# Performance work log

Measured on AMD Instinct MI355X. Metric: run time of the kernel, lower is better.

The kernel has to match this reference:

```python
import jax, jax.numpy as jnp
import numpy as np

SIZE = (256, 256, 256)   # volume shape (self.size)
N = 65536                # number of Gaussians
DIST = 3.0               # render cutoff distance
WIN = 7                  # static stencil width = 2*ceil(DIST)+1


def setup_inputs() -> dict:
    key = jax.random.key(0)
    k1, k2, k3 = jax.random.split(key, 3)
    # positions inside the volume
    pos = jax.random.uniform(k1, (3, N), minval=1.0, maxval=255.0)
    # per-Gaussian value
    value = jax.random.uniform(k2, (1, N), minval=0.1, maxval=1.0)
    # radii: diagonal radii in [1,3], off-diagonal cross terms ~ 0 (1e-5, as in create_guass)
    rdiag = jax.random.uniform(k3, (3, N), minval=1.0, maxval=3.0)
    off = jnp.full((N,), 1e-5, jnp.float32)
    # layout rows 4:10 -> [rx, rxy, rxz, ry, ryz, rz]
    r = jnp.stack([rdiag[0], off, off, rdiag[1], off, rdiag[2]], axis=0)
    paras = jnp.concatenate([pos, value, r], axis=0)  # [10, N]
    return {
        "paras": paras,
        "distance": jnp.float32(DIST),
        "thredhold": jnp.float32(1e-4),
    }


def _render(paras, distance, thredhold):
    # paras: [10, N] -> position [3,N], value [N], r [6,N]
    pos = paras[:3]
    val = paras[3]
    r = paras[4:]
    D0, D1, D2 = SIZE
    size_arr = jnp.array(SIZE, jnp.int32)

    # static local stencil offsets [W^3, 3]
    offs = jnp.stack(
        jnp.meshgrid(jnp.arange(WIN), jnp.arange(WIN), jnp.arange(WIN), indexing="ij"),
        axis=-1,
    ).reshape(-1, 3).astype(jnp.int32)

    corner = jnp.floor(pos.T).astype(jnp.int32) - (WIN // 2)   # [N, 3]
    vox = corner[:, None, :] + offs[None, :, :]                 # [N, W^3, 3] voxel coords
    d = vox.astype(paras.dtype) - pos.T[:, None, :]             # [N, W^3, 3] voxel - center
    dx, dy, dz = d[..., 0], d[..., 1], d[..., 2]

    rx, rxy, rxz, ry, ryz, rz = r  # each [N]
    # anisotropic quadratic form: diagonal radii + cross terms
    q = (
        (dx / rx[:, None]) ** 2
        + (dy / ry[:, None]) ** 2
        + (dz / rz[:, None]) ** 2
        + rxy[:, None] * dx * dy
        + rxz[:, None] * dx * dz
        + ryz[:, None] * dy * dz
    )
    w = jnp.exp(-0.5 * q)                                       # [N, W^3]

    dist2 = dx * dx + dy * dy + dz * dz
    inb = jnp.all((vox >= 0) & (vox < size_arr), axis=-1)
    mask = inb & (dist2 <= distance * distance) & (w > thredhold)
    contrib = jnp.where(mask, val[:, None] * w, 0.0)

    voxc = jnp.clip(vox, 0, size_arr - 1)
    flat = (voxc[..., 0] * D1 + voxc[..., 1]) * D2 + voxc[..., 2]
    out = jnp.zeros(D0 * D1 * D2, paras.dtype).at[flat.reshape(-1)].add(contrib.reshape(-1))
    return out.reshape(SIZE)


def reference(paras, distance, thredhold):
    return _render(paras, distance, thredhold)
```

## Files before the change

kernel.cpp:

```cpp
#include <hip/hip_runtime.h>

#define D0 256
#define D1 256
#define D2 256
#define NPTS 65536
#define HALF 3

#define TX 32
#define TY 16
#define TZ 16
#define NTILES 2048
#define TILE_VOX (TX * TY * TZ)

#define BLK 512
#define WPB 8
#define CAP 256

#define WS_COUNTS 0
#define WS_PREP   2048
#define WS_LIST   (WS_PREP + NPTS * 12)
#define FULL_INTS  (WS_LIST + NTILES * CAP)
#define WS_LIST_NP 2048
#define SMALL_INTS (WS_LIST_NP + NTILES * CAP)

struct OffTable { unsigned v[256]; };

constexpr OffTable make_table() {
    OffTable t{};
    int m[7] = {9, 4, 1, 0, 0, 1, 4};
    int n = 0;
    for (int i = 0; i < 7; i++)
        for (int j = 0; j < 7; j++)
            for (int k = 0; k < 7; k++)
                if (m[i] + m[j] + m[k] <= 9)
                    t.v[n++] = (unsigned)(i | (j << 8) | (k << 16));
    for (; n < 256; n++)
        t.v[n] = (unsigned)(100 | (100 << 8) | (100 << 16));
    return t;
}

__device__ __constant__ OffTable g_tab = make_table();

struct PP { float fx, fy, fz, val, ix, iy, iz, D, E, F; int pack; };

template<bool PREP>
__device__ __forceinline__ PP load_pt(const float* __restrict__ paras,
                                      const float* __restrict__ prep, int pidx) {
    PP P;
    if constexpr (PREP) {
        const float4* p4 = (const float4*)prep + pidx * 3;
        float4 a = p4[0], b4 = p4[1], c4 = p4[2];
        P.fx = a.x;  P.fy = a.y;  P.fz = a.z;  P.val = a.w;
        P.ix = b4.x; P.iy = b4.y; P.iz = b4.z; P.D = b4.w;
        P.E = c4.x;  P.F = c4.y;  P.pack = __float_as_int(c4.z);
    } else {
        float px = paras[pidx], py = paras[NPTS + pidx], pz = paras[2 * NPTS + pidx];
        P.val = paras[3 * NPTS + pidx];
        float rx  = paras[4 * NPTS + pidx], rxy = paras[5 * NPTS + pidx];
        float rxz = paras[6 * NPTS + pidx], ry  = paras[7 * NPTS + pidx];
        float ryz = paras[8 * NPTS + pidx], rz  = paras[9 * NPTS + pidx];
        int cx = (int)floorf(px) - HALF;
        int cy = (int)floorf(py) - HALF;
        int cz = (int)floorf(pz) - HALF;
        P.fx = (float)cx - px; P.fy = (float)cy - py; P.fz = (float)cz - pz;
        P.ix = __fdividef(1.f, rx); P.iy = __fdividef(1.f, ry);
        P.iz = __fdividef(1.f, rz);
        P.D = rxy; P.E = rxz; P.F = ryz;
        P.pack = (cx + 8) | ((cy + 8) << 10) | ((cz + 8) << 20);
    }
    return P;
}

__global__ __launch_bounds__(256)
void bin_kernel(const float* __restrict__ paras, int* __restrict__ ws,
                float* __restrict__ prep, int do_prep, int list_off) {
    int t = blockIdx.x * 256 + threadIdx.x;
    int p = t >> 3, j = t & 7;

    float px = paras[p], py = paras[NPTS + p], pz = paras[2 * NPTS + p];
    int cx = (int)floorf(px) - HALF;
    int cy = (int)floorf(py) - HALF;
    int cz = (int)floorf(pz) - HALF;

    if (do_prep && j == 0) {
        float val = paras[3 * NPTS + p];
        float rx  = paras[4 * NPTS + p], rxy = paras[5 * NPTS + p];
        float rxz = paras[6 * NPTS + p], ry  = paras[7 * NPTS + p];
        float ryz = paras[8 * NPTS + p], rz  = paras[9 * NPTS + p];
        int pack = (cx + 8) | ((cy + 8) << 10) | ((cz + 8) << 20);
        float4* o = (float4*)prep + p * 3;
        o[0] = make_float4((float)cx - px, (float)cy - py, (float)cz - pz, val);
        o[1] = make_float4(__fdividef(1.f, rx), __fdividef(1.f, ry),
                           __fdividef(1.f, rz), rxy);
        o[2] = make_float4(rxz, ryz, __int_as_float(pack), 0.f);
    }

    int xlo = max(cx, 0), xhi = min(cx + 6, D0 - 1);
    int ylo = max(cy, 0), yhi = min(cy + 6, D1 - 1);
    int zlo = max(cz, 0), zhi = min(cz + 6, D2 - 1);
    int txa = xlo >> 5, txb = xhi >> 5;
    int tya = ylo >> 4, tyb = yhi >> 4;
    int tza = zlo >> 4, tzb = zhi >> 4;

    bool dup = ((j & 1) && txb == txa) ||
               ((j & 2) && tyb == tya) ||
               ((j & 4) && tzb == tza);
    if (!dup) {
        int tx = (j & 1) ? txb : txa;
        int ty = (j & 2) ? tyb : tya;
        int tz = (j & 4) ? tzb : tza;
        int tt = (tx << 8) | (ty << 4) | tz;
        int slot = atomicAdd(&ws[WS_COUNTS + tt], 1);
        if (slot < CAP) ws[list_off + tt * CAP + slot] = p;
    }
}

template<bool PREP>
__global__ __launch_bounds__(512)
void tile_splat(const float* __restrict__ paras,
                const float* __restrict__ prep,
                const float* __restrict__ dist_p,
                const float* __restrict__ thr_p,
                const int* __restrict__ ws, int list_off,
                float* __restrict__ out) {
    __shared__ float acc[TILE_VOX];

    const int b   = blockIdx.x;
    const int tzi = b & 15, tyi = (b >> 4) & 15, txi = b >> 8;
    const int X0 = txi * TX, Y0 = tyi * TY, Z0 = tzi * TZ;
    const int tid = threadIdx.x;
    const int wid = tid >> 6, lane = tid & 63;

    int   oiv[4], ojv[4], okv[4];
    float foi[4], foj[4], fok[4];
#pragma unroll
    for (int t = 0; t < 4; t++) {
        unsigned pk = g_tab.v[t * 64 + lane];
        oiv[t] = pk & 255; ojv[t] = (pk >> 8) & 255; okv[t] = (int)(pk >> 16);
        foi[t] = (float)oiv[t]; foj[t] = (float)ojv[t]; fok[t] = (float)okv[t];
    }

    float4* acc4 = (float4*)acc;
    for (int q = tid; q < TILE_VOX / 4; q += BLK)
        acc4[q] = make_float4(0.f, 0.f, 0.f, 0.f);
    __syncthreads();

    const int n = min(ws[WS_COUNTS + b], CAP);
    const int lbase = list_off + b * CAP;
    const float dist  = dist_p[0];
    const float thr   = thr_p[0];
    const float d2max = dist * dist;

    int i = wid;
    PP cur;
    if (i < n) {
        int pidx = __builtin_amdgcn_readfirstlane(ws[lbase + i]);
        cur = load_pt<PREP>(paras, prep, pidx);
    }
    while (i < n) {
        int inext = i + WPB;
        PP nxt = cur;
        if (inext < n) {
            int pidx2 = __builtin_amdgcn_readfirstlane(ws[lbase + inext]);
            nxt = load_pt<PREP>(paras, prep, pidx2);
        }

        int pk  = cur.pack;
        int vx0 = (pk & 1023) - 8 - X0;
        int vy0 = ((pk >> 10) & 1023) - 8 - Y0;
        int vz0 = (pk >> 20) - 8 - Z0;

#pragma unroll
        for (int t = 0; t < 4; t++) {
            int vx = vx0 + oiv[t], vy = vy0 + ojv[t], vz = vz0 + okv[t];
            float dx = cur.fx + foi[t];
            float dy = cur.fy + foj[t];
            float dz = cur.fz + fok[t];
            float d2 = dx * dx + dy * dy + dz * dz;

            bool pass = ((unsigned)vx < (unsigned)TX) &
                        ((unsigned)vy < (unsigned)TY) &
                        ((unsigned)vz < (unsigned)TZ) &
                        (d2 <= d2max);
            if (pass) {
                float ax = dx * cur.ix, ay = dy * cur.iy, az = dz * cur.iz;
                float q = ax * ax + ay * ay + az * az
                        + cur.D * dx * dy + cur.E * dx * dz + cur.F * dy * dz;
                float w = __expf(-0.5f * q);
                if (w > thr)
                    atomicAdd(&acc[(vx << 8) | (vy << 4) | vz], cur.val * w);
            }
        }
        cur = nxt;
        i = inext;
    }
    __syncthreads();

    for (int q = tid; q < TILE_VOX / 4; q += BLK) {
        int vz = (q & 3) << 2;
        int vy = (q >> 2) & 15;
        int vx = q >> 6;
        *(float4*)&out[((X0 + vx) * D1 + (Y0 + vy)) * D2 + Z0 + vz] = acc4[q];
    }
}

__global__ __launch_bounds__(256)
void zero_kernel(float4* __restrict__ out, int n4) {
    int i = blockIdx.x * blockDim.x + threadIdx.x;
    int stride = gridDim.x * blockDim.x;
    for (; i < n4; i += stride)
        out[i] = make_float4(0.f, 0.f, 0.f, 0.f);
}

__global__ __launch_bounds__(256)
void splat_fallback(const float* __restrict__ paras,
                    const float* __restrict__ dist_p,
                    const float* __restrict__ thr_p,
                    float* __restrict__ out) {
    int wave = (blockIdx.x * blockDim.x + threadIdx.x) >> 6;
    int lane = threadIdx.x & 63;
    int p = __builtin_amdgcn_readfirstlane(wave);

    const int N = NPTS;
    float px  = paras[0 * N + p], py  = paras[1 * N + p], pz  = paras[2 * N + p];
    float val = paras[3 * N + p];
    float rx  = paras[4 * N + p], rxy = paras[5 * N + p], rxz = paras[6 * N + p];
    float ry  = paras[7 * N + p], ryz = paras[8 * N + p], rz  = paras[9 * N + p];

    float dist = dist_p[0], thr = thr_p[0];
    float d2max = dist * dist;

    int cx = (int)floorf(px) - HALF;
    int cy = (int)floorf(py) - HALF;
    int cz = (int)floorf(pz) - HALF;
    float fx = (float)cx - px, fy = (float)cy - py, fz = (float)cz - pz;
    float irx = __fdividef(1.f, rx), iry = __fdividef(1.f, ry),
          irz = __fdividef(1.f, rz);

#pragma unroll
    for (int t = 0; t < 4; t++) {
        unsigned pk = g_tab.v[t * 64 + lane];
        int oi = pk & 255, oj = (pk >> 8) & 255, ok = pk >> 16;
        int vx = cx + oi, vy = cy + oj, vz = cz + ok;
        float dx = fx + (float)oi, dy = fy + (float)oj, dz = fz + (float)ok;
        float d2 = dx * dx + dy * dy + dz * dz;
        bool inb = ((unsigned)vx < (unsigned)D0) &
                   ((unsigned)vy < (unsigned)D1) &
                   ((unsigned)vz < (unsigned)D2);
        if (inb && d2 <= d2max) {
            float ax = dx * irx, ay = dy * iry, az = dz * irz;
            float q = ax * ax + ay * ay + az * az
                    + rxy * dx * dy + rxz * dx * dz + ryz * dy * dz;
            float w = __expf(-0.5f * q);
            if (w > thr)
                atomicAdd(&out[(vx << 16) + (vy << 8) + vz], val * w);
        }
    }
}

extern "C" void kernel_launch(void* const* d_in, const int* in_sizes, int n_in,
                              void* d_out, int out_size, void* d_ws, size_t ws_size,
                              hipStream_t stream) {
    const float* paras  = (const float*)d_in[0];
    const float* dist_p = (const float*)d_in[1];
    const float* thr_p  = (const float*)d_in[2];
    float* out = (float*)d_out;
    int* ws = (int*)d_ws;
    float* prep = (float*)(ws + WS_PREP);

    if (ws_size >= (size_t)FULL_INTS * 4) {
        hipMemsetAsync(ws, 0, NTILES * sizeof(int), stream);
        bin_kernel<<<NPTS * 8 / 256, 256, 0, stream>>>(paras, ws, prep, 1, WS_LIST);
        tile_splat<true><<<NTILES, BLK, 0, stream>>>(paras, prep, dist_p, thr_p,
                                                     ws, WS_LIST, out);
    } else if (ws_size >= (size_t)SMALL_INTS * 4) {
        hipMemsetAsync(ws, 0, NTILES * sizeof(int), stream);
        bin_kernel<<<NPTS * 8 / 256, 256, 0, stream>>>(paras, ws, prep, 0, WS_LIST_NP);
        tile_splat<false><<<NTILES, BLK, 0, stream>>>(paras, prep, dist_p, thr_p,
                                                      ws, WS_LIST_NP, out);
    } else {
        zero_kernel<<<4096, 256, 0, stream>>>((float4*)out, out_size / 4);
        splat_fallback<<<NPTS / 4, 256, 0, stream>>>(paras, dist_p, thr_p, out);
    }
}
```

Before: 140.7 us.

## Replace atomic tile binning with per-tile ballot scan over all points

Drops the atomic binning pass and its per-tile index lists. A light prep kernel now writes a packed corner word and preprocessed parameters for each point. Each tile block then scans every point's packed corner, picks the ones touching its tile with a wave ballot, and splats them into shared memory. This removes the memset, the global atomics and the fixed per-tile capacity, but every block now reads the full point array, so total read traffic grows a lot. The intermediate workspace fallback path is also removed.

```diff
diff --git a/kernel.cpp b/kernel.cpp
--- a/kernel.cpp
+++ b/kernel.cpp
@@ -13,15 +13,11 @@
 #define TILE_VOX (TX * TY * TZ)
 
 #define BLK 512
-#define WPB 8
-#define CAP 256
-
-#define WS_COUNTS 0
-#define WS_PREP   2048
-#define WS_LIST   (WS_PREP + NPTS * 12)
-#define FULL_INTS  (WS_LIST + NTILES * CAP)
-#define WS_LIST_NP 2048
-#define SMALL_INTS (WS_LIST_NP + NTILES * CAP)
+#define PTS_PER_WAVE (NPTS / 8)
+
+#define WS_HOME   0
+#define WS_PREP   NPTS
+#define FULL_INTS (NPTS + NPTS * 12)
 
 struct OffTable { unsigned v[256]; };
 
@@ -43,85 +39,42 @@
 
 struct PP { float fx, fy, fz, val, ix, iy, iz, D, E, F; int pack; };
 
-template<bool PREP>
-__device__ __forceinline__ PP load_pt(const float* __restrict__ paras,
-                                      const float* __restrict__ prep, int pidx) {
+__device__ __forceinline__ PP load_pt(const float* __restrict__ prep, int pidx) {
     PP P;
-    if constexpr (PREP) {
-        const float4* p4 = (const float4*)prep + pidx * 3;
-        float4 a = p4[0], b4 = p4[1], c4 = p4[2];
-        P.fx = a.x;  P.fy = a.y;  P.fz = a.z;  P.val = a.w;
-        P.ix = b4.x; P.iy = b4.y; P.iz = b4.z; P.D = b4.w;
-        P.E = c4.x;  P.F = c4.y;  P.pack = __float_as_int(c4.z);
-    } else {
-        float px = paras[pidx], py = paras[NPTS + pidx], pz = paras[2 * NPTS + pidx];
-        P.val = paras[3 * NPTS + pidx];
-        float rx  = paras[4 * NPTS + pidx], rxy = paras[5 * NPTS + pidx];
-        float rxz = paras[6 * NPTS + pidx], ry  = paras[7 * NPTS + pidx];
-        float ryz = paras[8 * NPTS + pidx], rz  = paras[9 * NPTS + pidx];
-        int cx = (int)floorf(px) - HALF;
-        int cy = (int)floorf(py) - HALF;
-        int cz = (int)floorf(pz) - HALF;
-        P.fx = (float)cx - px; P.fy = (float)cy - py; P.fz = (float)cz - pz;
-        P.ix = __fdividef(1.f, rx); P.iy = __fdividef(1.f, ry);
-        P.iz = __fdividef(1.f, rz);
-        P.D = rxy; P.E = rxz; P.F = ryz;
-        P.pack = (cx + 8) | ((cy + 8) << 10) | ((cz + 8) << 20);
-    }
+    const float4* p4 = (const float4*)prep + pidx * 3;
+    float4 a = p4[0], b4 = p4[1], c4 = p4[2];
+    P.fx = a.x;  P.fy = a.y;  P.fz = a.z;  P.val = a.w;
+    P.ix = b4.x; P.iy = b4.y; P.iz = b4.z; P.D = b4.w;
+    P.E = c4.x;  P.F = c4.y;  P.pack = __float_as_int(c4.z);
     return P;
 }
 
 __global__ __launch_bounds__(256)
-void bin_kernel(const float* __restrict__ paras, int* __restrict__ ws,
-                float* __restrict__ prep, int do_prep, int list_off) {
-    int t = blockIdx.x * 256 + threadIdx.x;
-    int p = t >> 3, j = t & 7;
-
+void prep_kernel(const float* __restrict__ paras, int* __restrict__ ws) {
+    int p = blockIdx.x * 256 + threadIdx.x;
     float px = paras[p], py = paras[NPTS + p], pz = paras[2 * NPTS + p];
     int cx = (int)floorf(px) - HALF;
     int cy = (int)floorf(py) - HALF;
     int cz = (int)floorf(pz) - HALF;
 
-    if (do_prep && j == 0) {
-        float val = paras[3 * NPTS + p];
-        float rx  = paras[4 * NPTS + p], rxy = paras[5 * NPTS + p];
-        float rxz = paras[6 * NPTS + p], ry  = paras[7 * NPTS + p];
-        float ryz = paras[8 * NPTS + p], rz  = paras[9 * NPTS + p];
-        int pack = (cx + 8) | ((cy + 8) << 10) | ((cz + 8) << 20);
-        float4* o = (float4*)prep + p * 3;
-        o[0] = make_float4((float)cx - px, (float)cy - py, (float)cz - pz, val);
-        o[1] = make_float4(__fdividef(1.f, rx), __fdividef(1.f, ry),
-                           __fdividef(1.f, rz), rxy);
-        o[2] = make_float4(rxz, ryz, __int_as_float(pack), 0.f);
-    }
-
-    int xlo = max(cx, 0), xhi = min(cx + 6, D0 - 1);
-    int ylo = max(cy, 0), yhi = min(cy + 6, D1 - 1);
-    int zlo = max(cz, 0), zhi = min(cz + 6, D2 - 1);
-    int txa = xlo >> 5, txb = xhi >> 5;
-    int tya = ylo >> 4, tyb = yhi >> 4;
-    int tza = zlo >> 4, tzb = zhi >> 4;
-
-    bool dup = ((j & 1) && txb == txa) ||
-               ((j & 2) && tyb == tya) ||
-               ((j & 4) && tzb == tza);
-    if (!dup) {
-        int tx = (j & 1) ? txb : txa;
-        int ty = (j & 2) ? tyb : tya;
-        int tz = (j & 4) ? tzb : tza;
-        int tt = (tx << 8) | (ty << 4) | tz;
-        int slot = atomicAdd(&ws[WS_COUNTS + tt], 1);
-        if (slot < CAP) ws[list_off + tt * CAP + slot] = p;
-    }
-}
-
-template<bool PREP>
+    float val = paras[3 * NPTS + p];
+    float rx  = paras[4 * NPTS + p], rxy = paras[5 * NPTS + p];
+    float rxz = paras[6 * NPTS + p], ry  = paras[7 * NPTS + p];
+    float ryz = paras[8 * NPTS + p], rz  = paras[9 * NPTS + p];
+    int pack = (cx + 8) | ((cy + 8) << 10) | ((cz + 8) << 20);
+
+    ws[WS_HOME + p] = pack;
+    float4* o = (float4*)(ws + WS_PREP) + p * 3;
+    o[0] = make_float4((float)cx - px, (float)cy - py, (float)cz - pz, val);
+    o[1] = make_float4(__fdividef(1.f, rx), __fdividef(1.f, ry),
+                       __fdividef(1.f, rz), rxy);
+    o[2] = make_float4(rxz, ryz, __int_as_float(pack), 0.f);
+}
+
 __global__ __launch_bounds__(512)
-void tile_splat(const float* __restrict__ paras,
-                const float* __restrict__ prep,
-                const float* __restrict__ dist_p,
+void scan_splat(const float* __restrict__ dist_p,
                 const float* __restrict__ thr_p,
-                const int* __restrict__ ws, int list_off,
+                const int* __restrict__ ws,
                 float* __restrict__ out) {
     __shared__ float acc[TILE_VOX];
 
@@ -145,54 +98,56 @@
         acc4[q] = make_float4(0.f, 0.f, 0.f, 0.f);
     __syncthreads();
 
-    const int n = min(ws[WS_COUNTS + b], CAP);
-    const int lbase = list_off + b * CAP;
     const float dist  = dist_p[0];
     const float thr   = thr_p[0];
     const float d2max = dist * dist;
-
-    int i = wid;
-    PP cur;
-    if (i < n) {
-        int pidx = __builtin_amdgcn_readfirstlane(ws[lbase + i]);
-        cur = load_pt<PREP>(paras, prep, pidx);
-    }
-    while (i < n) {
-        int inext = i + WPB;
-        PP nxt = cur;
-        if (inext < n) {
-            int pidx2 = __builtin_amdgcn_readfirstlane(ws[lbase + inext]);
-            nxt = load_pt<PREP>(paras, prep, pidx2);
-        }
-
-        int pk  = cur.pack;
-        int vx0 = (pk & 1023) - 8 - X0;
-        int vy0 = ((pk >> 10) & 1023) - 8 - Y0;
-        int vz0 = (pk >> 20) - 8 - Z0;
+    const float* prep = (const float*)(ws + WS_PREP);
+    const int* home = ws + WS_HOME;
+
+    const int bx = X0 + 2, by = Y0 + 2, bz = Z0 + 2;
+
+    const int wstart = wid * PTS_PER_WAVE;
+    for (int it = 0; it < PTS_PER_WAVE; it += 64) {
+        const int wbase = wstart + it;
+        int hp = home[wbase + lane];
+        bool hit = ((unsigned)((hp & 1023) - bx) <= 37u) &
+                   ((unsigned)(((hp >> 10) & 1023) - by) <= 21u) &
+                   ((unsigned)((hp >> 20) - bz) <= 21u);
+
+        unsigned long long m = __ballot(hit);
+        while (m) {
+            int l = __ffsll(m) - 1;
+            m &= m - 1;
+            int pidx = __builtin_amdgcn_readfirstlane(wbase + l);
+            PP cur = load_pt(prep, pidx);
+
+            int pk  = cur.pack;
+            int vx0 = (pk & 1023) - 8 - X0;
+            int vy0 = ((pk >> 10) & 1023) - 8 - Y0;
+            int vz0 = (pk >> 20) - 8 - Z0;
 
 #pragma unroll
-        for (int t = 0; t < 4; t++) {
-            int vx = vx0 + oiv[t], vy = vy0 + ojv[t], vz = vz0 + okv[t];
-            float dx = cur.fx + foi[t];
-            float dy = cur.fy + foj[t];
-            float dz = cur.fz + fok[t];
-            float d2 = dx * dx + dy * dy + dz * dz;
-
-            bool pass = ((unsigned)vx < (unsigned)TX) &
-                        ((unsigned)vy < (unsigned)TY) &
-                        ((unsigned)vz < (unsigned)TZ) &
-                        (d2 <= d2max);
-            if (pass) {
-                float ax = dx * cur.ix, ay = dy * cur.iy, az = dz * cur.iz;
-                float q = ax * ax + ay * ay + az * az
-                        + cur.D * dx * dy + cur.E * dx * dz + cur.F * dy * dz;
-                float w = __expf(-0.5f * q);
-                if (w > thr)
-                    atomicAdd(&acc[(vx << 8) | (vy << 4) | vz], cur.val * w);
+            for (int t = 0; t < 4; t++) {
+                int vx = vx0 + oiv[t], vy = vy0 + ojv[t], vz = vz0 + okv[t];
+                float dx = cur.fx + foi[t];
+                float dy = cur.fy + foj[t];
+                float dz = cur.fz + fok[t];
+                float d2 = dx * dx + dy * dy + dz * dz;
+
+                bool pass = ((unsigned)vx < (unsigned)TX) &
+                            ((unsigned)vy < (unsigned)TY) &
+                            ((unsigned)vz < (unsigned)TZ) &
+                            (d2 <= d2max);
+                if (pass) {
+                    float ax = dx * cur.ix, ay = dy * cur.iy, az = dz * cur.iz;
+                    float q = ax * ax + ay * ay + az * az
+                            + cur.D * dx * dy + cur.E * dx * dz + cur.F * dy * dz;
+                    float w = __expf(-0.5f * q);
+                    if (w > thr)
+                        atomicAdd(&acc[(vx << 8) | (vy << 4) | vz], cur.val * w);
+                }
             }
         }
-        cur = nxt;
-        i = inext;
     }
     __syncthreads();
 
@@ -266,18 +221,10 @@
     const float* thr_p  = (const float*)d_in[2];
     float* out = (float*)d_out;
     int* ws = (int*)d_ws;
-    float* prep = (float*)(ws + WS_PREP);
 
     if (ws_size >= (size_t)FULL_INTS * 4) {
-        hipMemsetAsync(ws, 0, NTILES * sizeof(int), stream);
-        bin_kernel<<<NPTS * 8 / 256, 256, 0, stream>>>(paras, ws, prep, 1, WS_LIST);
-        tile_splat<true><<<NTILES, BLK, 0, stream>>>(paras, prep, dist_p, thr_p,
-                                                     ws, WS_LIST, out);
-    } else if (ws_size >= (size_t)SMALL_INTS * 4) {
-        hipMemsetAsync(ws, 0, NTILES * sizeof(int), stream);
-        bin_kernel<<<NPTS * 8 / 256, 256, 0, stream>>>(paras, ws, prep, 0, WS_LIST_NP);
-        tile_splat<false><<<NTILES, BLK, 0, stream>>>(paras, prep, dist_p, thr_p,
-                                                      ws, WS_LIST_NP, out);
+        prep_kernel<<<NPTS / 256, 256, 0, stream>>>(paras, ws);
+        scan_splat<<<NTILES, BLK, 0, stream>>>(dist_p, thr_p, ws, out);
     } else {
         zero_kernel<<<4096, 256, 0, stream>>>((float4*)out, out_size / 4);
         splat_fallback<<<NPTS / 4, 256, 0, stream>>>(paras, dist_p, thr_p, out);
```

New measurement: 179.3 us. +27.4%, slower.
